# Kernel optimization log

Hardware: AMD Instinct MI355X
Metric: run time of the kernel (lower is better)

## Reference

```python
import jax, jax.numpy as jnp
import numpy as np

N_INT4, N_INT8, K, GROUP = 6144, 2048, 8192, 128
N_TOTAL = N_INT4 + N_INT8
M = 16


def setup_inputs() -> dict:
    key = jax.random.key(0)
    ks = jax.random.split(key, 8)
    x = jax.random.normal(ks[0], (M, K), jnp.float32)
    # uint4 weights: values 0..15 (stored int32)
    w_int4 = jax.random.randint(ks[1], (N_INT4, K), 0, 16, jnp.int32)
    # group-wise scales [N_int4, K//group_size]
    s_int4 = jax.random.uniform(ks[2], (N_INT4, K // GROUP), jnp.float32, minval=0.005, maxval=0.02)
    # int8 weights stored in offset-128 form (w_int8 + 128 -> 0..255), as pack_for_marlin builds
    w_uint8 = jax.random.randint(ks[3], (N_INT8, K), 0, 256, jnp.int32)
    # per-channel int8 scales
    s_int8 = jax.random.uniform(ks[4], (N_INT8,), jnp.float32, minval=0.005, maxval=0.02)
    awq_scales = jax.random.uniform(ks[5], (K,), jnp.float32, minval=0.5, maxval=2.0)
    bias = jax.random.normal(ks[6], (N_TOTAL,), jnp.float32) * 0.01
    inv_perm = jax.random.permutation(ks[7], N_TOTAL).astype(jnp.int32)
    return dict(x=x, w_int4=w_int4, s_int4=s_int4, w_uint8=w_uint8, s_int8=s_int8,
                awq_scales=awq_scales, bias=bias, inv_perm=inv_perm, group_size=GROUP)


def reference(x, w_int4, s_int4, w_uint8, s_int8, awq_scales, bias, inv_perm, group_size):
    dt = x.dtype
    k = x.shape[-1]
    # AWQ input scaling (unfused path: x / awq_scales)
    x2 = x.reshape(-1, k) / awq_scales[None, :]
    sum_x = jnp.sum(x2, axis=1, keepdims=True)  # [M, 1]

    # Marlin uint4b8 dequant: (q - 8) * scale, group-wise scales for int4 rows
    s4_k = jnp.repeat(s_int4, group_size, axis=1)            # [N4, K]
    W4 = (w_int4.astype(dt) - 8.0) * s4_k                    # [N4, K]

    # int8 rows split into high/low nibbles with scales 16*s and s
    high = (w_uint8 >> 4) & 15
    low = w_uint8 & 15
    Wh = (high.astype(dt) - 8.0) * (16.0 * s_int8)[:, None]  # [N8, K]
    Wl = (low.astype(dt) - 8.0) * s_int8[:, None]            # [N8, K]

    Wc = jnp.concatenate([W4, Wh, Wl], axis=0)               # [N4+2*N8, K]
    y = x2 @ Wc.T                                            # marlin_gemm equivalent

    n4 = W4.shape[0]
    n8 = s_int8.shape[0]
    y4 = y[:, :n4]
    # int8 reconstruction: y_high + y_low + 8*s_int8*sum_x  == s_int8 * (x @ w_int8^T)
    y8 = y[:, n4:n4 + n8] + y[:, n4 + n8:] + (8.0 * s_int8)[None, :] * sum_x
    y_out = jnp.concatenate([y4, y8], axis=-1)[:, inv_perm] + bias[None, :]
    return y_out.reshape(*x.shape[:-1], n4 + n8)
```

## Files before the change

### kernel.cpp

```cpp
#include <hip/hip_runtime.h>
#include <hip/hip_bf16.h>

constexpr int K    = 8192;
constexpr int N4   = 6144;
constexpr int N8   = 2048;
constexpr int NT   = N4 + N8;
constexpr int NG   = K / 128;
constexpr int WSTR = 258;

typedef short  short8  __attribute__((ext_vector_type(8)));
typedef float  floatx4 __attribute__((ext_vector_type(4)));
typedef __attribute__((address_space(1))) void gas_t;
typedef __attribute__((address_space(3))) void las_t;

__device__ inline short f2bf(float f) {
    __hip_bfloat16 h = __float2bfloat16(f);
    return __builtin_bit_cast(short, h);
}

__device__ __forceinline__ void dma16(const void* g, void* l) {
    __builtin_amdgcn_global_load_lds((gas_t*)g, (las_t*)l, 16, 0, 0);
}

__global__ void prep_kernel(const float* __restrict__ x,
                            const float* __restrict__ awq,
                            const int*   __restrict__ inv_perm,
                            const float* __restrict__ bias,
                            short* __restrict__ x2bf,
                            int*   __restrict__ fwd,
                            float* __restrict__ out) {
    const int tid  = blockIdx.x * blockDim.x + threadIdx.x;
    const int c    = tid >> 9;
    const int rem  = tid & 511;
    const int lane = rem >> 3;
    const int j    = rem & 7;
    const int m    = lane & 15;
    const int k    = c * 32 + (lane >> 4) * 8 + j;
    x2bf[tid] = f2bf(x[m * K + k] / awq[k]);
    out[tid]  = bias[tid & (NT - 1)];
    if (tid < NT) fwd[inv_perm[tid]] = tid;
}

__device__ __forceinline__ floatx4 chunk_mfma(int4 wa, int4 wb, short8 xv,
                                              float off, floatx4 cin) {
    short8 bf;
    bf[0] = f2bf((float)wa.x + off);
    bf[1] = f2bf((float)wa.y + off);
    bf[2] = f2bf((float)wa.z + off);
    bf[3] = f2bf((float)wa.w + off);
    bf[4] = f2bf((float)wb.x + off);
    bf[5] = f2bf((float)wb.y + off);
    bf[6] = f2bf((float)wb.z + off);
    bf[7] = f2bf((float)wb.w + off);
    return __builtin_amdgcn_mfma_f32_16x16x32_bf16(xv, bf, cin, 0, 0, 0);
}

__global__ __launch_bounds__(256)
void qgemv_kernel(const short* __restrict__ xf,
                  const int*   __restrict__ w4,
                  const float* __restrict__ s4,
                  const int*   __restrict__ w8,
                  const float* __restrict__ s8,
                  const int*   __restrict__ fwd,
                  float* __restrict__ out) {
    __shared__ int   wbuf[2][16 * WSTR];
    __shared__ float red[4][256];

    const int t    = threadIdx.x;
    const int lane = t & 63;
    const int w    = t >> 6;
    const int tile = blockIdx.x >> 1;
    const int spl  = blockIdx.x & 1;
    const int nb   = tile * 16;
    const int i    = lane & 15;
    const int q    = lane >> 4;
    const int row  = nb + i;

    const bool  is4 = (nb < N4);
    const float off = is4 ? -8.f : -128.f;
    const float s8row = is4 ? 0.f : s8[row - N4];
    const int   kb  = spl * 4096;

    const int* wbase = is4 ? (w4 + (size_t)nb * K) : (w8 + (size_t)(nb - N4) * K);

    floatx4 acc = {0.f, 0.f, 0.f, 0.f};

    #pragma unroll
    for (int a = 0; a < 4; ++a) {
        const int r = w + 4 * a;
        dma16(wbase + (size_t)r * K + kb + lane * 4, &wbuf[0][r * WSTR]);
    }

    #pragma unroll 1
    for (int it = 0; it < 16; ++it) {
        const int nxt = (it + 1 < 16) ? it + 1 : 15;
        #pragma unroll
        for (int a = 0; a < 4; ++a) {
            const int r = w + 4 * a;
            dma16(wbase + (size_t)r * K + kb + nxt * 256 + lane * 4,
                  &wbuf[(it + 1) & 1][r * WSTR]);
        }

        const int   g  = spl * 32 + it * 2 + (w >> 1);
        const float sg = is4 ? s4[(size_t)row * NG + g] : s8row;

        __syncthreads();

        const int* wb = &wbuf[it & 1][0];
        floatx4 gacc = {0.f, 0.f, 0.f, 0.f};
        #pragma unroll
        for (int cc = 0; cc < 2; ++cc) {
            const int c   = 2 * w + cc;
            const int4 wv0 = *(const int4*)(wb + i * WSTR + c * 32 + q * 8);
            const int4 wv1 = *(const int4*)(wb + i * WSTR + c * 32 + q * 8 + 4);
            const short8 xv = *(const short8*)(xf + (size_t)(spl * 128 + it * 8 + c) * 512
                                               + lane * 8);
            gacc = chunk_mfma(wv0, wv1, xv, off, gacc);
        }
        acc[0] += sg * gacc[0]; acc[1] += sg * gacc[1];
        acc[2] += sg * gacc[2]; acc[3] += sg * gacc[3];

        __syncthreads();
    }

    #pragma unroll
    for (int r = 0; r < 4; ++r)
        red[w][(q * 4 + r) * 16 + i] = acc[r];
    __syncthreads();

    if (t < 256) {
        const float v = red[0][t] + red[1][t] + red[2][t] + red[3][t];
        const int m  = t >> 4;
        const int i2 = t & 15;
        const int d  = fwd[nb + i2];
        unsafeAtomicAdd(&out[(size_t)m * NT + d], v);
    }
}

extern "C" void kernel_launch(void* const* d_in, const int* in_sizes, int n_in,
                              void* d_out, int out_size, void* d_ws, size_t ws_size,
                              hipStream_t stream) {
    const float* x        = (const float*)d_in[0];
    const int*   w_int4   = (const int*)  d_in[1];
    const float* s_int4   = (const float*)d_in[2];
    const int*   w_uint8  = (const int*)  d_in[3];
    const float* s_int8   = (const float*)d_in[4];
    const float* awq      = (const float*)d_in[5];
    const float* bias     = (const float*)d_in[6];
    const int*   inv_perm = (const int*)  d_in[7];

    short* x2bf = (short*)d_ws;
    int*   fwd  = (int*)((char*)d_ws + (size_t)16 * K * sizeof(short));

    prep_kernel<<<(16 * K) / 256, 256, 0, stream>>>(x, awq, inv_perm, bias,
                                                    x2bf, fwd, (float*)d_out);
    qgemv_kernel<<<1024, 256, 0, stream>>>(x2bf, w_int4, s_int4,
                                           w_uint8, s_int8, fwd,
                                           (float*)d_out);
}
```

Before: 338.0 us.

## Repack weights into MFMA-ordered nibble/byte layout and read it directly

```diff
diff --git a/kernel.cpp b/kernel.cpp
--- a/kernel.cpp
+++ b/kernel.cpp
@@ -6,29 +6,23 @@
 constexpr int N8   = 2048;
 constexpr int NT   = N4 + N8;
 constexpr int NG   = K / 128;
-constexpr int WSTR = 258;
 
 typedef short  short8  __attribute__((ext_vector_type(8)));
 typedef float  floatx4 __attribute__((ext_vector_type(4)));
-typedef __attribute__((address_space(1))) void gas_t;
-typedef __attribute__((address_space(3))) void las_t;
 
-__device__ inline short f2bf(float f) {
+__device__ __forceinline__ short f2bf(float f) {
     __hip_bfloat16 h = __float2bfloat16(f);
     return __builtin_bit_cast(short, h);
 }
-
-__device__ __forceinline__ void dma16(const void* g, void* l) {
-    __builtin_amdgcn_global_load_lds((gas_t*)g, (las_t*)l, 16, 0, 0);
+__device__ __forceinline__ short ibf(float f) {
+    return (short)(__builtin_bit_cast(unsigned, f) >> 16);
 }
 
 __global__ void prep_kernel(const float* __restrict__ x,
                             const float* __restrict__ awq,
                             const int*   __restrict__ inv_perm,
-                            const float* __restrict__ bias,
                             short* __restrict__ x2bf,
-                            int*   __restrict__ fwd,
-                            float* __restrict__ out) {
+                            int*   __restrict__ fwd) {
     const int tid  = blockIdx.x * blockDim.x + threadIdx.x;
     const int c    = tid >> 9;
     const int rem  = tid & 511;
@@ -37,90 +31,125 @@
     const int m    = lane & 15;
     const int k    = c * 32 + (lane >> 4) * 8 + j;
     x2bf[tid] = f2bf(x[m * K + k] / awq[k]);
-    out[tid]  = bias[tid & (NT - 1)];
     if (tid < NT) fwd[inv_perm[tid]] = tid;
 }
 
-__device__ __forceinline__ floatx4 chunk_mfma(int4 wa, int4 wb, short8 xv,
-                                              float off, floatx4 cin) {
-    short8 bf;
-    bf[0] = f2bf((float)wa.x + off);
-    bf[1] = f2bf((float)wa.y + off);
-    bf[2] = f2bf((float)wa.z + off);
-    bf[3] = f2bf((float)wa.w + off);
-    bf[4] = f2bf((float)wb.x + off);
-    bf[5] = f2bf((float)wb.y + off);
-    bf[6] = f2bf((float)wb.z + off);
-    bf[7] = f2bf((float)wb.w + off);
-    return __builtin_amdgcn_mfma_f32_16x16x32_bf16(xv, bf, cin, 0, 0, 0);
+__global__ __launch_bounds__(256)
+void repack4_kernel(const int* __restrict__ w4, unsigned* __restrict__ p4) {
+    __shared__ unsigned lt[16][17];
+    const int j    = threadIdx.x;
+    const int tile = blockIdx.x >> 6;
+    const int gb   = blockIdx.x & 63;
+    const int rl   = j >> 4;
+    const int kl   = j & 15;
+    const size_t t_in = (size_t)(tile * 16 + rl) * 1024 + gb * 16 + kl;
+    const int4 a = *(const int4*)(w4 + t_in * 8);
+    const int4 b = *(const int4*)(w4 + t_in * 8 + 4);
+    lt[rl][kl] = (unsigned)(a.x & 15)        | ((unsigned)(a.y & 15) << 4)
+               | ((unsigned)(a.z & 15) << 8) | ((unsigned)(a.w & 15) << 12)
+               | ((unsigned)(b.x & 15) << 16)| ((unsigned)(b.y & 15) << 20)
+               | ((unsigned)(b.z & 15) << 24)| ((unsigned)(b.w & 15) << 28);
+    __syncthreads();
+    const int cL = j >> 6, rem = j & 63, q = rem >> 4, i = rem & 15;
+    p4[(size_t)tile * 16384 + gb * 256 + j] = lt[i][cL * 4 + q];
+}
+
+__global__ __launch_bounds__(256)
+void repack8_kernel(const int* __restrict__ w8, uint2* __restrict__ p8) {
+    __shared__ uint2 lt[16][17];
+    const int j    = threadIdx.x;
+    const int tile = blockIdx.x >> 6;
+    const int gb   = blockIdx.x & 63;
+    const int rl   = j >> 4;
+    const int kl   = j & 15;
+    const size_t t_in = (size_t)(tile * 16 + rl) * 1024 + gb * 16 + kl;
+    const int4 a = *(const int4*)(w8 + t_in * 8);
+    const int4 b = *(const int4*)(w8 + t_in * 8 + 4);
+    uint2 d;
+    d.x = (unsigned)(a.x & 255)         | ((unsigned)(a.y & 255) << 8)
+        | ((unsigned)(a.z & 255) << 16) | ((unsigned)(a.w & 255) << 24);
+    d.y = (unsigned)(b.x & 255)         | ((unsigned)(b.y & 255) << 8)
+        | ((unsigned)(b.z & 255) << 16) | ((unsigned)(b.w & 255) << 24);
+    lt[rl][kl] = d;
+    __syncthreads();
+    const int cL = j >> 6, rem = j & 63, q = rem >> 4, i = rem & 15;
+    p8[(size_t)tile * 16384 + gb * 256 + j] = lt[i][cL * 4 + q];
+}
+
+__device__ __forceinline__ short8 dq4(unsigned v) {
+    short8 r;
+    #pragma unroll
+    for (int j = 0; j < 8; ++j)
+        r[j] = ibf((float)((v >> (4 * j)) & 15u) - 8.f);
+    return r;
+}
+__device__ __forceinline__ short8 dq8(uint2 d) {
+    short8 r;
+    #pragma unroll
+    for (int j = 0; j < 4; ++j) {
+        r[j]     = ibf((float)((d.x >> (8 * j)) & 255u) - 128.f);
+        r[4 + j] = ibf((float)((d.y >> (8 * j)) & 255u) - 128.f);
+    }
+    return r;
 }
 
 __global__ __launch_bounds__(256)
 void qgemv_kernel(const short* __restrict__ xf,
-                  const int*   __restrict__ w4,
+                  const unsigned* __restrict__ p4,
                   const float* __restrict__ s4,
-                  const int*   __restrict__ w8,
+                  const uint2* __restrict__ p8,
                   const float* __restrict__ s8,
                   const int*   __restrict__ fwd,
+                  const float* __restrict__ bias,
                   float* __restrict__ out) {
-    __shared__ int   wbuf[2][16 * WSTR];
     __shared__ float red[4][256];
 
     const int t    = threadIdx.x;
     const int lane = t & 63;
     const int w    = t >> 6;
-    const int tile = blockIdx.x >> 1;
-    const int spl  = blockIdx.x & 1;
+    const int tile = blockIdx.x;
     const int nb   = tile * 16;
     const int i    = lane & 15;
     const int q    = lane >> 4;
     const int row  = nb + i;
 
-    const bool  is4 = (nb < N4);
-    const float off = is4 ? -8.f : -128.f;
-    const float s8row = is4 ? 0.f : s8[row - N4];
-    const int   kb  = spl * 4096;
-
-    const int* wbase = is4 ? (w4 + (size_t)nb * K) : (w8 + (size_t)(nb - N4) * K);
-
     floatx4 acc = {0.f, 0.f, 0.f, 0.f};
 
-    #pragma unroll
-    for (int a = 0; a < 4; ++a) {
-        const int r = w + 4 * a;
-        dma16(wbase + (size_t)r * K + kb + lane * 4, &wbuf[0][r * WSTR]);
-    }
-
-    #pragma unroll 1
-    for (int it = 0; it < 16; ++it) {
-        const int nxt = (it + 1 < 16) ? it + 1 : 15;
-        #pragma unroll
-        for (int a = 0; a < 4; ++a) {
-            const int r = w + 4 * a;
-            dma16(wbase + (size_t)r * K + kb + nxt * 256 + lane * 4,
-                  &wbuf[(it + 1) & 1][r * WSTR]);
+    if (nb < N4) {
+        const unsigned* pw = p4 + (size_t)tile * 16384;
+        const float*    sp = s4 + (size_t)row * NG;
+        #pragma unroll 1
+        for (int cg = 0; cg < 16; ++cg) {
+            const int c0 = w * 64 + cg * 4;
+            floatx4 g = {0.f, 0.f, 0.f, 0.f};
+            #pragma unroll
+            for (int cc = 0; cc < 4; ++cc) {
+                const int c = c0 + cc;
+                const unsigned v  = pw[(size_t)c * 64 + lane];
+                const short8   xv = *(const short8*)(xf + (size_t)c * 512 + lane * 8);
+                g = __builtin_amdgcn_mfma_f32_16x16x32_bf16(xv, dq4(v), g, 0, 0, 0);
+            }
+            const float sg = sp[c0 >> 2];
+            acc[0] += sg * g[0]; acc[1] += sg * g[1];
+            acc[2] += sg * g[2]; acc[3] += sg * g[3];
         }
-
-        const int   g  = spl * 32 + it * 2 + (w >> 1);
-        const float sg = is4 ? s4[(size_t)row * NG + g] : s8row;
-
-        __syncthreads();
-
-        const int* wb = &wbuf[it & 1][0];
-        floatx4 gacc = {0.f, 0.f, 0.f, 0.f};
-        #pragma unroll
-        for (int cc = 0; cc < 2; ++cc) {
-            const int c   = 2 * w + cc;
-            const int4 wv0 = *(const int4*)(wb + i * WSTR + c * 32 + q * 8);
-            const int4 wv1 = *(const int4*)(wb + i * WSTR + c * 32 + q * 8 + 4);
-            const short8 xv = *(const short8*)(xf + (size_t)(spl * 128 + it * 8 + c) * 512
-                                               + lane * 8);
-            gacc = chunk_mfma(wv0, wv1, xv, off, gacc);
+    } else {
+        const uint2* pw  = p8 + (size_t)(tile - N4 / 16) * 16384;
+        const float  s8r = s8[row - N4];
+        #pragma unroll 1
+        for (int cg = 0; cg < 16; ++cg) {
+            const int c0 = w * 64 + cg * 4;
+            floatx4 g = {0.f, 0.f, 0.f, 0.f};
+            #pragma unroll
+            for (int cc = 0; cc < 4; ++cc) {
+                const int c = c0 + cc;
+                const uint2  v  = pw[(size_t)c * 64 + lane];
+                const short8 xv = *(const short8*)(xf + (size_t)c * 512 + lane * 8);
+                g = __builtin_amdgcn_mfma_f32_16x16x32_bf16(xv, dq8(v), g, 0, 0, 0);
+            }
+            acc[0] += s8r * g[0]; acc[1] += s8r * g[1];
+            acc[2] += s8r * g[2]; acc[3] += s8r * g[3];
         }
-        acc[0] += sg * gacc[0]; acc[1] += sg * gacc[1];
-        acc[2] += sg * gacc[2]; acc[3] += sg * gacc[3];
-
-        __syncthreads();
     }
 
     #pragma unroll
@@ -132,8 +161,9 @@
         const float v = red[0][t] + red[1][t] + red[2][t] + red[3][t];
         const int m  = t >> 4;
         const int i2 = t & 15;
-        const int d  = fwd[nb + i2];
-        unsafeAtomicAdd(&out[(size_t)m * NT + d], v);
+        const int n  = nb + i2;
+        const int d  = fwd[n];
+        out[(size_t)m * NT + d] = v + bias[d];
     }
 }
 
@@ -149,12 +179,15 @@
     const float* bias     = (const float*)d_in[6];
     const int*   inv_perm = (const int*)  d_in[7];
 
-    short* x2bf = (short*)d_ws;
-    int*   fwd  = (int*)((char*)d_ws + (size_t)16 * K * sizeof(short));
+    char* ws = (char*)d_ws;
+    short*    x2bf = (short*)ws;
+    int*      fwd  = (int*)(ws + 262144);
+    unsigned* p4   = (unsigned*)(ws + 294912);
+    uint2*    p8   = (uint2*)(ws + 294912 + 25165824);
 
-    prep_kernel<<<(16 * K) / 256, 256, 0, stream>>>(x, awq, inv_perm, bias,
-                                                    x2bf, fwd, (float*)d_out);
-    qgemv_kernel<<<1024, 256, 0, stream>>>(x2bf, w_int4, s_int4,
-                                           w_uint8, s_int8, fwd,
-                                           (float*)d_out);
+    prep_kernel<<<512, 256, 0, stream>>>(x, awq, inv_perm, x2bf, fwd);
+    repack4_kernel<<<24576, 256, 0, stream>>>(w_int4, p4);
+    repack8_kernel<<<8192, 256, 0, stream>>>(w_uint8, p8);
+    qgemv_kernel<<<512, 256, 0, stream>>>(x2bf, p4, s_int4, p8, s_int8,
+                                          fwd, bias, (float*)d_out);
 }
```

Measured after the change: 343.5 us. Within noise of the previous version (+1.6%).
